# Performance work log

Hardware: AMD Instinct MI355X
Metric: run time of the kernel (lower is better)

The kernel has to match this reference:

```python
import jax, jax.numpy as jnp
import numpy as np

B, M, W, C, NN, J, ED, EMB = 8, 4096, 128, 32, 16, 4, 5, 2
EPS = 1e-5


def setup_inputs() -> dict:
    key = jax.random.key(0)
    ks = jax.random.split(key, 30)
    s = 0.05
    x = jax.random.normal(ks[0], (B, M, W), jnp.float32)
    pseudo = jax.random.normal(ks[1], (M * NN, EMB), jnp.float32)
    # structured indices: row r scatters its NN attention weights into row r of the m x m matrix
    nbr = jax.random.randint(ks[2], (M, NN), 0, M)
    L_idx = (jnp.arange(M)[:, None] * M + nbr).reshape(-1).astype(jnp.int32)
    inp = dict(x=x, pseudo=pseudo, L_idx=L_idx)
    inp['edge_w'] = jax.random.normal(ks[3], (ED, EMB), jnp.float32) * s
    inp['edge_b'] = jnp.zeros((ED,), jnp.float32)
    # Gaussian mixture params per layer (J components, encode_dim each); reset_parameters -> N(0,1)
    inp['mu0'] = jax.random.normal(ks[4], (J, ED), jnp.float32)
    inp['sigma0'] = jax.random.normal(ks[5], (J, ED), jnp.float32)
    inp['mu1'] = jax.random.normal(ks[6], (J, ED), jnp.float32)
    inp['sigma1'] = jax.random.normal(ks[7], (J, ED), jnp.float32)
    # layer 0: W -> C ; layer 1: C -> C
    inp['l1w0'] = jax.random.normal(ks[8], (C, W), jnp.float32) * s
    inp['l1b0'] = jnp.zeros((C,), jnp.float32)
    inp['l2w0'] = jax.random.normal(ks[9], (C, W), jnp.float32) * s
    inp['l2b0'] = jnp.zeros((C,), jnp.float32)
    inp['l1w1'] = jax.random.normal(ks[10], (C, C), jnp.float32) * s
    inp['l1b1'] = jnp.zeros((C,), jnp.float32)
    inp['l2w1'] = jax.random.normal(ks[11], (C, C), jnp.float32) * s
    inp['l2b1'] = jnp.zeros((C,), jnp.float32)
    inp['bn_g0'] = jnp.ones((C,), jnp.float32)
    inp['bn_b0'] = jnp.zeros((C,), jnp.float32)
    inp['bn_g1'] = jnp.ones((C,), jnp.float32)
    inp['bn_b1'] = jnp.zeros((C,), jnp.float32)
    inp['fc1w'] = jax.random.normal(ks[12], (256, M * C), jnp.float32) * 0.005
    inp['fc1b'] = jnp.zeros((256,), jnp.float32)
    inp['fc2w'] = jax.random.normal(ks[13], (53, 256), jnp.float32) * s
    inp['fc2b'] = jnp.zeros((53,), jnp.float32)
    return inp


def _get_L(pseudo, L_idx, edge_w, edge_b, mu, sigma, dtype):
    # Gaussian-mixture edge attention: u^T diag(sigma) u per component, summed, exp(-0.5 *)
    emb = pseudo @ edge_w.T + edge_b                      # (E, ED), E = M*NN
    u = emb[None, :, :] - mu[:, None, :]                  # (J, E, ED)
    q = jnp.sum(u * u * sigma[:, None, :], axis=-1)       # (J, E)
    w = jnp.sum(jnp.exp(-0.5 * q), axis=0)                # (E,)
    attn = jax.nn.softmax(w.reshape(M, NN), axis=1).reshape(-1)
    return jnp.zeros(M * M, dtype).at[L_idx].set(attn).reshape(M, M)


def _layer(x, L, w1, b1, w2, b2, g, bb):
    Lx = jnp.einsum('mn,bnf->bmf', L, x)                  # graph conv
    h = Lx @ w1.T + b1 + x @ w2.T + b2                    # (B, M, C)
    # BatchNorm1d (training mode): stats over batch and node dims, biased variance
    mean = jnp.mean(h, axis=(0, 1))
    var = jnp.var(h, axis=(0, 1))
    h = (h - mean) * jax.lax.rsqrt(var + EPS) * g + bb
    return jax.nn.relu(h)


def reference(x, pseudo, L_idx, edge_w, edge_b, mu0, sigma0, mu1, sigma1,
              l1w0, l1b0, l2w0, l2b0, l1w1, l1b1, l2w1, l2b1,
              bn_g0, bn_b0, bn_g1, bn_b1, fc1w, fc1b, fc2w, fc2b):
    L0 = _get_L(pseudo, L_idx, edge_w, edge_b, mu0, sigma0, x.dtype)
    h = _layer(x, L0, l1w0, l1b0, l2w0, l2b0, bn_g0, bn_b0)
    L1 = _get_L(pseudo, L_idx, edge_w, edge_b, mu1, sigma1, x.dtype)
    h = _layer(h, L1, l1w1, l1b1, l2w1, l2b1, bn_g1, bn_b1)
    flat = h.reshape(B, M * C)
    out = jax.nn.relu(flat @ fc1w.T + fc1b)               # dropout = identity (eval)
    return out @ fc2w.T + fc2b                            # (B, 53)
```

## Files before the change

### kernel.cpp

```cpp
#include <hip/hip_runtime.h>

#define B_ 8
#define M_ 4096
#define W_ 128
#define C_ 32
#define NN_ 16

typedef short s16x8 __attribute__((ext_vector_type(8)));
typedef float f32x4 __attribute__((ext_vector_type(4)));

static __device__ __forceinline__ unsigned short f2bf(float f) {
  unsigned u = __builtin_bit_cast(unsigned, f);
  u = u + 0x7FFFu + ((u >> 16) & 1u);
  return (unsigned short)(u >> 16);
}
static __device__ __forceinline__ s16x8 cvt8v(float4 a, float4 b) {
  s16x8 r;
  r[0] = (short)f2bf(a.x); r[1] = (short)f2bf(a.y);
  r[2] = (short)f2bf(a.z); r[3] = (short)f2bf(a.w);
  r[4] = (short)f2bf(b.x); r[5] = (short)f2bf(b.y);
  r[6] = (short)f2bf(b.z); r[7] = (short)f2bf(b.w);
  return r;
}
static __device__ __forceinline__ float safeexp(float a) {
  return expf(fminf(a, 87.f));
}

__global__ void poison_kernel(float* __restrict__ out, int n, float val) {
  int t = blockIdx.x * blockDim.x + threadIdx.x;
  if (t < n) out[t] = val;
}

__global__ __launch_bounds__(256) void init_kernel(
    float* __restrict__ fc1acc, const float* __restrict__ fc1b,
    float* __restrict__ bn) {
  int g = blockIdx.x * 256 + threadIdx.x;
  if (g < 2048) fc1acc[g] = fc1b[g & 255];
  else if (g < 34816) bn[g - 2048] = 0.f;
}

__global__ __launch_bounds__(256) void attn_kernel(
    const float* __restrict__ pseudo, const int* __restrict__ Lidx,
    const float* __restrict__ edge_w, const float* __restrict__ edge_b,
    const float* __restrict__ mu0, const float* __restrict__ sg0,
    const float* __restrict__ mu1, const float* __restrict__ sg1,
    float* __restrict__ we0, float* __restrict__ we1, int* __restrict__ colb) {
  int m = blockIdx.x * 256 + threadIdx.x;
  if (m >= M_) return;
  float w0[NN_], w1[NN_];
  int col[NN_];
#pragma unroll
  for (int n = 0; n < NN_; n++) {
    int e = m * NN_ + n;
    float p0 = pseudo[e * 2], p1 = pseudo[e * 2 + 1];
    float emb[5];
#pragma unroll
    for (int d = 0; d < 5; d++)
      emb[d] = p0 * edge_w[d * 2] + p1 * edge_w[d * 2 + 1] + edge_b[d];
    float a0 = 0.f, a1 = 0.f;
#pragma unroll
    for (int j = 0; j < 4; j++) {
      float qa = 0.f, qb = 0.f;
#pragma unroll
      for (int d = 0; d < 5; d++) {
        float u0 = emb[d] - mu0[j * 5 + d];
        qa += u0 * u0 * sg0[j * 5 + d];
        float u1 = emb[d] - mu1[j * 5 + d];
        qb += u1 * u1 * sg1[j * 5 + d];
      }
      a0 += safeexp(-0.5f * qa);
      a1 += safeexp(-0.5f * qb);
    }
    w0[n] = a0; w1[n] = a1;
    col[n] = Lidx[e] % M_;
  }
  float mx0 = w0[0], mx1 = w1[0];
#pragma unroll
  for (int n = 1; n < NN_; n++) { mx0 = fmaxf(mx0, w0[n]); mx1 = fmaxf(mx1, w1[n]); }
  float s0 = 0.f, s1 = 0.f;
#pragma unroll
  for (int n = 0; n < NN_; n++) {
    w0[n] = safeexp(w0[n] - mx0); s0 += w0[n];
    w1[n] = safeexp(w1[n] - mx1); s1 += w1[n];
  }
  float r0 = 1.f / s0, r1 = 1.f / s1;
#pragma unroll
  for (int n = 0; n < NN_; n++) {
    bool last = true;
#pragma unroll
    for (int n2 = n + 1; n2 < NN_; n2++)
      if (col[n2] == col[n]) last = false;
    int e = m * NN_ + n;
    we0[e] = last ? w0[n] * r0 : 0.f;
    we1[e] = last ? w1[n] * r1 : 0.f;
    colb[e] = col[n];
  }
}

__global__ __launch_bounds__(256) void proj0_kernel(
    const float* __restrict__ x, const float* __restrict__ l1w0,
    const float* __restrict__ l2w0, float* __restrict__ G) {
  int lane = threadIdx.x & 63, wave = threadIdx.x >> 6;
  int l16 = lane & 15, quad = lane >> 4;
  int tile = blockIdx.x * 4 + wave;
  s16x8 bf[4][4];
#pragma unroll
  for (int kit = 0; kit < 4; kit++) {
#pragma unroll
    for (int ct = 0; ct < 4; ct++) {
      int out = ct * 16 + l16;
      const float* src = (out < 32 ? l1w0 + out * 128 : l2w0 + (out - 32) * 128)
                         + kit * 32 + quad * 8;
      bf[kit][ct] = cvt8v(*(const float4*)src, *(const float4*)(src + 4));
    }
  }
  f32x4 acc[4];
#pragma unroll
  for (int ct = 0; ct < 4; ct++) acc[ct] = (f32x4){0.f, 0.f, 0.f, 0.f};
  int row = tile * 16 + l16;
  const float* xr = x + (size_t)row * 128 + quad * 8;
#pragma unroll
  for (int kit = 0; kit < 4; kit++) {
    const float* ap = xr + kit * 32;
    s16x8 a = cvt8v(*(const float4*)ap, *(const float4*)(ap + 4));
#pragma unroll
    for (int ct = 0; ct < 4; ct++)
      acc[ct] = __builtin_amdgcn_mfma_f32_16x16x32_bf16(a, bf[kit][ct], acc[ct], 0, 0, 0);
  }
  int rbase = tile * 16 + quad * 4;
#pragma unroll
  for (int ct = 0; ct < 4; ct++)
#pragma unroll
    for (int i = 0; i < 4; i++)
      G[(size_t)(rbase + i) * 64 + ct * 16 + l16] = acc[ct][i];
}

__global__ __launch_bounds__(256) void conv_kernel(
    const float* __restrict__ G,
    const float* __restrict__ we, const int* __restrict__ colb,
    const float* __restrict__ b1c, const float* __restrict__ b2c,
    float* __restrict__ h, float* __restrict__ bns, float* __restrict__ bnq) {
  __shared__ float s_we[8][16];
  __shared__ int   s_cn[8][16];
  __shared__ float s_s[32], s_q[32];
  int tid = threadIdx.x;
  if (tid < 128) {
    int row = tid >> 4, nn = tid & 15;
    int m = (blockIdx.x * 8 + row) & 4095;
    s_we[row][nn] = we[m * 16 + nn];
    s_cn[row][nn] = colb[m * 16 + nn];
  } else if (tid < 160) {
    s_s[tid - 128] = 0.f;
    s_q[tid - 128] = 0.f;
  }
  __syncthreads();
  int row = tid >> 5, c = tid & 31;
  int r = blockIdx.x * 8 + row;
  int b = r >> 12;
  const float* Gb = G + ((size_t)b << 18);
  float acc = 0.f;
#pragma unroll
  for (int nn = 0; nn < NN_; nn++)
    acc += s_we[row][nn] * Gb[s_cn[row][nn] * 64 + c];
  float hv = acc + G[(size_t)r * 64 + 32 + c] + b1c[c] + b2c[c];
  h[(size_t)r * 32 + c] = hv;
  atomicAdd(&s_s[c], hv);
  atomicAdd(&s_q[c], hv * hv);
  __syncthreads();
  if (tid < 32) {
    int slot = blockIdx.x & 255;
    atomicAdd(&bns[tid * 256 + slot], s_s[tid]);
    atomicAdd(&bnq[tid * 256 + slot], s_q[tid]);
  }
}

__global__ __launch_bounds__(256) void bnfin_kernel(
    const float* __restrict__ bns, const float* __restrict__ bnq,
    const float* __restrict__ g, const float* __restrict__ bb,
    float* __restrict__ scale, float* __restrict__ shift) {
  __shared__ float red[2][8][32];
  int tid = threadIdx.x;
  int c = tid & 31, part = tid >> 5;
  float s = 0.f, q = 0.f;
#pragma unroll 8
  for (int i = 0; i < 32; i++) {
    s += bns[c * 256 + part * 32 + i];
    q += bnq[c * 256 + part * 32 + i];
  }
  red[0][part][c] = s;
  red[1][part][c] = q;
  __syncthreads();
  if (tid < 32) {
    float S = 0.f, Q = 0.f;
#pragma unroll
    for (int p = 0; p < 8; p++) { S += red[0][p][tid]; Q += red[1][p][tid]; }
    float mean = S * (1.f / 32768.f);
    float var = fmaxf(Q * (1.f / 32768.f) - mean * mean, 0.f);
    float sc = g[tid] * rsqrtf(var + 1e-5f);
    scale[tid] = sc;
    shift[tid] = bb[tid] - mean * sc;
  }
}

__global__ __launch_bounds__(256) void proj1_kernel(
    const float* __restrict__ h0, const float* __restrict__ sc0,
    const float* __restrict__ l1w1, const float* __restrict__ l2w1,
    float* __restrict__ G) {
  int lane = threadIdx.x & 63, wave = threadIdx.x >> 6;
  int l16 = lane & 15, quad = lane >> 4;
  int tile = blockIdx.x * 4 + wave;
  s16x8 bf[4];
#pragma unroll
  for (int ct = 0; ct < 4; ct++) {
    int out = ct * 16 + l16;
    const float* src = (out < 32 ? l1w1 + out * 32 : l2w1 + (out - 32) * 32) + quad * 8;
    bf[ct] = cvt8v(*(const float4*)src, *(const float4*)(src + 4));
  }
  float scv[8], shv[8];
#pragma unroll
  for (int j = 0; j < 8; j++) {
    scv[j] = sc0[quad * 8 + j];
    shv[j] = sc0[32 + quad * 8 + j];
  }
  int row = tile * 16 + l16;
  const float* hr = h0 + (size_t)row * 32 + quad * 8;
  float4 hv0 = *(const float4*)hr;
  float4 hv1 = *(const float4*)(hr + 4);
  float av[8] = {hv0.x, hv0.y, hv0.z, hv0.w, hv1.x, hv1.y, hv1.z, hv1.w};
  s16x8 a;
#pragma unroll
  for (int j = 0; j < 8; j++)
    a[j] = (short)f2bf(fmaxf(av[j] * scv[j] + shv[j], 0.f));
  f32x4 acc[4];
#pragma unroll
  for (int ct = 0; ct < 4; ct++) {
    f32x4 z = {0.f, 0.f, 0.f, 0.f};
    acc[ct] = __builtin_amdgcn_mfma_f32_16x16x32_bf16(a, bf[ct], z, 0, 0, 0);
  }
  int rbase = tile * 16 + quad * 4;
#pragma unroll
  for (int ct = 0; ct < 4; ct++)
#pragma unroll
    for (int i = 0; i < 4; i++)
      G[(size_t)(rbase + i) * 64 + ct * 16 + l16] = acc[ct][i];
}

__global__ __launch_bounds__(256) void fc1_kernel(
    const float* __restrict__ h1, const float* __restrict__ sc1,
    const float* __restrict__ fc1w, float* __restrict__ fc1acc) {
  __shared__ short als[16 * 1024];
  int tid = threadIdx.x;
  int kc = blockIdx.x >> 2;
  int og = blockIdx.x & 3;
  size_t kbase = (size_t)kc << 10;
  for (int s = tid; s < 4096; s += 256) {
    int rowb = s >> 8;
    int k4 = (s & 255) << 2;
    short4 v4 = {0, 0, 0, 0};
    if (rowb < 8) {
      float4 hv = *(const float4*)(h1 + ((size_t)rowb << 17) + kbase + k4);
      int c = k4 & 31;
      float4 scv = *(const float4*)(sc1 + c);
      float4 shv = *(const float4*)(sc1 + 32 + c);
      v4.x = (short)f2bf(fmaxf(hv.x * scv.x + shv.x, 0.f));
      v4.y = (short)f2bf(fmaxf(hv.y * scv.y + shv.y, 0.f));
      v4.z = (short)f2bf(fmaxf(hv.z * scv.z + shv.z, 0.f));
      v4.w = (short)f2bf(fmaxf(hv.w * scv.w + shv.w, 0.f));
    }
    int byte = ((rowb << 11) + (k4 << 1)) ^ ((rowb & 7) << 4);
    *(short4*)((char*)als + byte) = v4;
  }
  __syncthreads();
  int lane = tid & 63, wave = tid >> 6;
  int l16 = lane & 15, quad = lane >> 4;
  const float* wrow = fc1w + (size_t)(og * 64 + wave * 16 + l16) * 131072
                      + kbase + quad * 8;
  int abase = (l16 << 11) + (quad << 4);
  int axor = (l16 & 7) << 4;
  f32x4 acc = {0.f, 0.f, 0.f, 0.f};
#pragma unroll 4
  for (int kk = 0; kk < 32; kk++) {
    const float* wp = wrow + kk * 32;
    s16x8 bfr = cvt8v(*(const float4*)wp, *(const float4*)(wp + 4));
    s16x8 afr = *(const s16x8*)((const char*)als + ((abase + (kk << 6)) ^ axor));
    acc = __builtin_amdgcn_mfma_f32_16x16x32_bf16(afr, bfr, acc, 0, 0, 0);
  }
  if (quad < 2) {
    int o = og * 64 + wave * 16 + l16;
#pragma unroll
    for (int i = 0; i < 4; i++)
      atomicAdd(&fc1acc[(quad * 4 + i) * 256 + o], acc[i]);
  }
}

__global__ void fc2_kernel(const float* __restrict__ fc1acc,
                           const float* __restrict__ fc2w,
                           const float* __restrict__ fc2b,
                           float* __restrict__ out) {
  int t = blockIdx.x * blockDim.x + threadIdx.x;
  if (t >= 424) return;
  int b = t / 53, j = t - b * 53;
  float s = fc2b[j];
  const float* fa = fc1acc + b * 256;
  const float* wr = fc2w + j * 256;
#pragma unroll 8
  for (int o = 0; o < 256; o++) s += fmaxf(fa[o], 0.f) * wr[o];
  out[t] = s;
}

extern "C" void kernel_launch(void* const* d_in, const int* in_sizes, int n_in,
                              void* d_out, int out_size, void* d_ws, size_t ws_size,
                              hipStream_t stream) {
  float* out = (float*)d_out;
  int bad = 0;
  if (n_in != 25) bad = 2;
  else if (in_sizes[0] != 4194304) bad = 3;
  else if (in_sizes[2] != 65536) bad = 4;
  else if (in_sizes[21] != 33554432) bad = 5;
  else if (out_size != 424) bad = 6;
  else if (ws_size < 13509120) bad = 1;
  if (bad) {
    poison_kernel<<<2, 256, 0, stream>>>(out, out_size, (float)bad * 1.0e6f);
    return;
  }

  const float* x      = (const float*)d_in[0];
  const float* pseudo = (const float*)d_in[1];
  const int*   Lidx   = (const int*)d_in[2];
  const float* edge_w = (const float*)d_in[3];
  const float* edge_b = (const float*)d_in[4];
  const float* mu0    = (const float*)d_in[5];
  const float* sg0    = (const float*)d_in[6];
  const float* mu1    = (const float*)d_in[7];
  const float* sg1    = (const float*)d_in[8];
  const float* l1w0   = (const float*)d_in[9];
  const float* l1b0   = (const float*)d_in[10];
  const float* l2w0   = (const float*)d_in[11];
  const float* l2b0   = (const float*)d_in[12];
  const float* l1w1   = (const float*)d_in[13];
  const float* l1b1   = (const float*)d_in[14];
  const float* l2w1   = (const float*)d_in[15];
  const float* l2b1   = (const float*)d_in[16];
  const float* bng0   = (const float*)d_in[17];
  const float* bnb0   = (const float*)d_in[18];
  const float* bng1   = (const float*)d_in[19];
  const float* bnb1   = (const float*)d_in[20];
  const float* fc1w   = (const float*)d_in[21];
  const float* fc1b   = (const float*)d_in[22];
  const float* fc2w   = (const float*)d_in[23];
  const float* fc2b   = (const float*)d_in[24];

  char* Wp = (char*)d_ws;
  int*   colb   = (int*)  (Wp + 0);
  float* we0    = (float*)(Wp + 262144);
  float* we1    = (float*)(Wp + 524288);
  float* G      = (float*)(Wp + 786432);
  float* h0     = (float*)(Wp + 9175040);
  float* h1     = (float*)(Wp + 9175040);
  float* bn     = (float*)(Wp + 13369344);
  float* sc     = (float*)(Wp + 13500416);
  float* fc1acc = (float*)(Wp + 13500928);

  init_kernel<<<136, 256, 0, stream>>>(fc1acc, fc1b, bn);
  attn_kernel<<<16, 256, 0, stream>>>(pseudo, Lidx, edge_w, edge_b,
                                      mu0, sg0, mu1, sg1, we0, we1, colb);
  proj0_kernel<<<512, 256, 0, stream>>>(x, l1w0, l2w0, G);
  conv_kernel<<<4096, 256, 0, stream>>>(G, we0, colb, l1b0, l2b0,
                                        h0, bn, bn + 8192);
  bnfin_kernel<<<1, 256, 0, stream>>>(bn, bn + 8192, bng0, bnb0, sc, sc + 32);
  proj1_kernel<<<512, 256, 0, stream>>>(h0, sc, l1w1, l2w1, G);
  conv_kernel<<<4096, 256, 0, stream>>>(G, we1, colb, l1b1, l2b1,
                                        h1, bn + 16384, bn + 24576);
  bnfin_kernel<<<1, 256, 0, stream>>>(bn + 16384, bn + 24576, bng1, bnb1,
                                      sc + 64, sc + 96);
  fc1_kernel<<<512, 256, 0, stream>>>(h1, sc + 64, fc1w, fc1acc);
  fc2_kernel<<<2, 256, 0, stream>>>(fc1acc, fc2w, fc2b, out);
}
```

Measured before the change: 346.5 us.

## Fuse init/attn/proj0, fold BN finalize into consumers, prefetch fc1 weights, split fc1 K

Merges the init, attention and layer-0 projection kernels into one launch, and folds each BatchNorm finalize into the kernel that consumes it. Each block now recomputes the scale and shift redundantly, which removes the single-block kernels and their launch gaps. The second conv kernel also reads the whole 128 MB fc1 weight array through an empty asm sink so it lands in cache (L2/MALL) before fc1 runs. fc1 now uses twice as many blocks, each splitting K across wave pairs and combining them through LDS. The risks are extra memory traffic from the prefetch and repeated BN reductions in every block.

```diff
diff --git a/kernel.cpp b/kernel.cpp
--- a/kernel.cpp
+++ b/kernel.cpp
@@ -31,22 +31,13 @@
   if (t < n) out[t] = val;
 }
 
-__global__ __launch_bounds__(256) void init_kernel(
-    float* __restrict__ fc1acc, const float* __restrict__ fc1b,
-    float* __restrict__ bn) {
-  int g = blockIdx.x * 256 + threadIdx.x;
-  if (g < 2048) fc1acc[g] = fc1b[g & 255];
-  else if (g < 34816) bn[g - 2048] = 0.f;
-}
-
-__global__ __launch_bounds__(256) void attn_kernel(
-    const float* __restrict__ pseudo, const int* __restrict__ Lidx,
+
+static __device__ void attn_row(
+    int m, const float* __restrict__ pseudo, const int* __restrict__ Lidx,
     const float* __restrict__ edge_w, const float* __restrict__ edge_b,
     const float* __restrict__ mu0, const float* __restrict__ sg0,
     const float* __restrict__ mu1, const float* __restrict__ sg1,
     float* __restrict__ we0, float* __restrict__ we1, int* __restrict__ colb) {
-  int m = blockIdx.x * 256 + threadIdx.x;
-  if (m >= M_) return;
   float w0[NN_], w1[NN_];
   int col[NN_];
 #pragma unroll
@@ -97,35 +88,29 @@
   }
 }
 
-__global__ __launch_bounds__(256) void proj0_kernel(
-    const float* __restrict__ x, const float* __restrict__ l1w0,
+static __device__ void proj0_tile(
+    int blk, int tid, const float* __restrict__ x, const float* __restrict__ l1w0,
     const float* __restrict__ l2w0, float* __restrict__ G) {
-  int lane = threadIdx.x & 63, wave = threadIdx.x >> 6;
+  int lane = tid & 63, wave = tid >> 6;
   int l16 = lane & 15, quad = lane >> 4;
-  int tile = blockIdx.x * 4 + wave;
-  s16x8 bf[4][4];
+  int tile = blk * 4 + wave;
+  f32x4 acc[4];
+#pragma unroll
+  for (int ct = 0; ct < 4; ct++) acc[ct] = (f32x4){0.f, 0.f, 0.f, 0.f};
+  int row = tile * 16 + l16;
+  const float* xr = x + (size_t)row * 128 + quad * 8;
 #pragma unroll
   for (int kit = 0; kit < 4; kit++) {
+    const float* ap = xr + kit * 32;
+    s16x8 a = cvt8v(*(const float4*)ap, *(const float4*)(ap + 4));
 #pragma unroll
     for (int ct = 0; ct < 4; ct++) {
       int out = ct * 16 + l16;
       const float* src = (out < 32 ? l1w0 + out * 128 : l2w0 + (out - 32) * 128)
                          + kit * 32 + quad * 8;
-      bf[kit][ct] = cvt8v(*(const float4*)src, *(const float4*)(src + 4));
+      s16x8 bf = cvt8v(*(const float4*)src, *(const float4*)(src + 4));
+      acc[ct] = __builtin_amdgcn_mfma_f32_16x16x32_bf16(a, bf, acc[ct], 0, 0, 0);
     }
-  }
-  f32x4 acc[4];
-#pragma unroll
-  for (int ct = 0; ct < 4; ct++) acc[ct] = (f32x4){0.f, 0.f, 0.f, 0.f};
-  int row = tile * 16 + l16;
-  const float* xr = x + (size_t)row * 128 + quad * 8;
-#pragma unroll
-  for (int kit = 0; kit < 4; kit++) {
-    const float* ap = xr + kit * 32;
-    s16x8 a = cvt8v(*(const float4*)ap, *(const float4*)(ap + 4));
-#pragma unroll
-    for (int ct = 0; ct < 4; ct++)
-      acc[ct] = __builtin_amdgcn_mfma_f32_16x16x32_bf16(a, bf[kit][ct], acc[ct], 0, 0, 0);
   }
   int rbase = tile * 16 + quad * 4;
 #pragma unroll
@@ -135,18 +120,19 @@
       G[(size_t)(rbase + i) * 64 + ct * 16 + l16] = acc[ct][i];
 }
 
-__global__ __launch_bounds__(256) void conv_kernel(
-    const float* __restrict__ G,
-    const float* __restrict__ we, const int* __restrict__ colb,
-    const float* __restrict__ b1c, const float* __restrict__ b2c,
-    float* __restrict__ h, float* __restrict__ bns, float* __restrict__ bnq) {
-  __shared__ float s_we[8][16];
-  __shared__ int   s_cn[8][16];
-  __shared__ float s_s[32], s_q[32];
-  int tid = threadIdx.x;
+static __device__ void conv_block(
+    int cb, int tid, char* smem,
+    const float* __restrict__ G, const float* __restrict__ we,
+    const int* __restrict__ colb, const float* __restrict__ b1c,
+    const float* __restrict__ b2c, float* __restrict__ h,
+    float* __restrict__ bns, float* __restrict__ bnq) {
+  float (*s_we)[16] = (float(*)[16])smem;
+  int   (*s_cn)[16] = (int(*)[16])(smem + 512);
+  float* s_s = (float*)(smem + 1024);
+  float* s_q = (float*)(smem + 1152);
   if (tid < 128) {
     int row = tid >> 4, nn = tid & 15;
-    int m = (blockIdx.x * 8 + row) & 4095;
+    int m = (cb * 8 + row) & 4095;
     s_we[row][nn] = we[m * 16 + nn];
     s_cn[row][nn] = colb[m * 16 + nn];
   } else if (tid < 160) {
@@ -155,7 +141,7 @@
   }
   __syncthreads();
   int row = tid >> 5, c = tid & 31;
-  int r = blockIdx.x * 8 + row;
+  int r = cb * 8 + row;
   int b = r >> 12;
   const float* Gb = G + ((size_t)b << 18);
   float acc = 0.f;
@@ -168,18 +154,17 @@
   atomicAdd(&s_q[c], hv * hv);
   __syncthreads();
   if (tid < 32) {
-    int slot = blockIdx.x & 255;
+    int slot = cb & 255;
     atomicAdd(&bns[tid * 256 + slot], s_s[tid]);
     atomicAdd(&bnq[tid * 256 + slot], s_q[tid]);
   }
 }
 
-__global__ __launch_bounds__(256) void bnfin_kernel(
-    const float* __restrict__ bns, const float* __restrict__ bnq,
+static __device__ void bnfin_local(
+    int tid, char* smem, const float* __restrict__ bns, const float* __restrict__ bnq,
     const float* __restrict__ g, const float* __restrict__ bb,
-    float* __restrict__ scale, float* __restrict__ shift) {
-  __shared__ float red[2][8][32];
-  int tid = threadIdx.x;
+    float* __restrict__ s_sc) {
+  float (*red)[8][32] = (float(*)[8][32])smem;
   int c = tid & 31, part = tid >> 5;
   float s = 0.f, q = 0.f;
 #pragma unroll 8
@@ -197,31 +182,19 @@
     float mean = S * (1.f / 32768.f);
     float var = fmaxf(Q * (1.f / 32768.f) - mean * mean, 0.f);
     float sc = g[tid] * rsqrtf(var + 1e-5f);
-    scale[tid] = sc;
-    shift[tid] = bb[tid] - mean * sc;
-  }
-}
-
-__global__ __launch_bounds__(256) void proj1_kernel(
-    const float* __restrict__ h0, const float* __restrict__ sc0,
+    s_sc[tid] = sc;
+    s_sc[32 + tid] = bb[tid] - mean * sc;
+  }
+  __syncthreads();
+}
+
+static __device__ void proj1_tile(
+    int blk, int tid, const float* __restrict__ h0, const float* __restrict__ sc0,
     const float* __restrict__ l1w1, const float* __restrict__ l2w1,
     float* __restrict__ G) {
-  int lane = threadIdx.x & 63, wave = threadIdx.x >> 6;
+  int lane = tid & 63, wave = tid >> 6;
   int l16 = lane & 15, quad = lane >> 4;
-  int tile = blockIdx.x * 4 + wave;
-  s16x8 bf[4];
-#pragma unroll
-  for (int ct = 0; ct < 4; ct++) {
-    int out = ct * 16 + l16;
-    const float* src = (out < 32 ? l1w1 + out * 32 : l2w1 + (out - 32) * 32) + quad * 8;
-    bf[ct] = cvt8v(*(const float4*)src, *(const float4*)(src + 4));
-  }
-  float scv[8], shv[8];
-#pragma unroll
-  for (int j = 0; j < 8; j++) {
-    scv[j] = sc0[quad * 8 + j];
-    shv[j] = sc0[32 + quad * 8 + j];
-  }
+  int tile = blk * 4 + wave;
   int row = tile * 16 + l16;
   const float* hr = h0 + (size_t)row * 32 + quad * 8;
   float4 hv0 = *(const float4*)hr;
@@ -229,13 +202,19 @@
   float av[8] = {hv0.x, hv0.y, hv0.z, hv0.w, hv1.x, hv1.y, hv1.z, hv1.w};
   s16x8 a;
 #pragma unroll
-  for (int j = 0; j < 8; j++)
-    a[j] = (short)f2bf(fmaxf(av[j] * scv[j] + shv[j], 0.f));
+  for (int j = 0; j < 8; j++) {
+    float scv = sc0[quad * 8 + j];
+    float shv = sc0[32 + quad * 8 + j];
+    a[j] = (short)f2bf(fmaxf(av[j] * scv + shv, 0.f));
+  }
   f32x4 acc[4];
 #pragma unroll
   for (int ct = 0; ct < 4; ct++) {
+    int out = ct * 16 + l16;
+    const float* src = (out < 32 ? l1w1 + out * 32 : l2w1 + (out - 32) * 32) + quad * 8;
+    s16x8 bf = cvt8v(*(const float4*)src, *(const float4*)(src + 4));
     f32x4 z = {0.f, 0.f, 0.f, 0.f};
-    acc[ct] = __builtin_amdgcn_mfma_f32_16x16x32_bf16(a, bf[ct], z, 0, 0, 0);
+    acc[ct] = __builtin_amdgcn_mfma_f32_16x16x32_bf16(a, bf, z, 0, 0, 0);
   }
   int rbase = tile * 16 + quad * 4;
 #pragma unroll
@@ -245,13 +224,94 @@
       G[(size_t)(rbase + i) * 64 + ct * 16 + l16] = acc[ct][i];
 }
 
-__global__ __launch_bounds__(256) void fc1_kernel(
-    const float* __restrict__ h1, const float* __restrict__ sc1,
+static __device__ void fc2_elem(
+    int t, const float* __restrict__ fc1acc, const float* __restrict__ fc2w,
+    const float* __restrict__ fc2b, float* __restrict__ out) {
+  int b = t / 53, j = t - b * 53;
+  float s = fc2b[j];
+  const float* fa = fc1acc + b * 256;
+  const float* wr = fc2w + j * 256;
+#pragma unroll 8
+  for (int o = 0; o < 256; o++) s += fmaxf(fa[o], 0.f) * wr[o];
+  out[t] = s;
+}
+
+
+__global__ __launch_bounds__(256) void k1_kernel(
+    const float* __restrict__ x, const float* __restrict__ l1w0,
+    const float* __restrict__ l2w0, float* __restrict__ G,
+    const float* __restrict__ pseudo, const int* __restrict__ Lidx,
+    const float* __restrict__ edge_w, const float* __restrict__ edge_b,
+    const float* __restrict__ mu0, const float* __restrict__ sg0,
+    const float* __restrict__ mu1, const float* __restrict__ sg1,
+    float* __restrict__ we0, float* __restrict__ we1, int* __restrict__ colb,
+    float* __restrict__ fc1acc, const float* __restrict__ fc1b,
+    float* __restrict__ bn) {
+  int bid = blockIdx.x, tid = threadIdx.x;
+  if (bid < 512) {
+    proj0_tile(bid, tid, x, l1w0, l2w0, G);
+  } else if (bid < 528) {
+    attn_row((bid - 512) * 256 + tid, pseudo, Lidx, edge_w, edge_b,
+             mu0, sg0, mu1, sg1, we0, we1, colb);
+  } else {
+    int g = (bid - 528) * 256 + tid;
+    if (g < 2048) fc1acc[g] = fc1b[g & 255];
+    else bn[g - 2048] = 0.f;
+  }
+}
+
+__global__ __launch_bounds__(256) void conv_kernel(
+    const float* __restrict__ G,
+    const float* __restrict__ we, const int* __restrict__ colb,
+    const float* __restrict__ b1c, const float* __restrict__ b2c,
+    float* __restrict__ h, float* __restrict__ bns, float* __restrict__ bnq) {
+  __shared__ char smem[1280];
+  conv_block(blockIdx.x, threadIdx.x, smem, G, we, colb, b1c, b2c, h, bns, bnq);
+}
+
+__global__ __launch_bounds__(256) void proj1bn_kernel(
+    const float* __restrict__ h0,
+    const float* __restrict__ bns, const float* __restrict__ bnq,
+    const float* __restrict__ g0, const float* __restrict__ b0,
+    const float* __restrict__ l1w1, const float* __restrict__ l2w1,
+    float* __restrict__ G) {
+  __shared__ char smem[2048];
+  __shared__ __align__(16) float s_sc[64];
+  bnfin_local(threadIdx.x, smem, bns, bnq, g0, b0, s_sc);
+  proj1_tile(blockIdx.x, threadIdx.x, h0, s_sc, l1w1, l2w1, G);
+}
+
+__global__ __launch_bounds__(256) void conv_pf_kernel(
+    const float* __restrict__ G,
+    const float* __restrict__ we, const int* __restrict__ colb,
+    const float* __restrict__ b1c, const float* __restrict__ b2c,
+    float* __restrict__ h, float* __restrict__ bns, float* __restrict__ bnq,
+    const float* __restrict__ fc1w) {
+  __shared__ char smem[1280];
+  conv_block(blockIdx.x, threadIdx.x, smem, G, we, colb, b1c, b2c, h, bns, bnq);
+  const float4* pw = (const float4*)fc1w;
+  int base = blockIdx.x * 2048 + threadIdx.x;
+  float a = 0.f;
+#pragma unroll
+  for (int j = 0; j < 8; j++) {
+    float4 v = pw[base + j * 256];
+    a += v.x + v.y + v.z + v.w;
+  }
+  asm volatile("" :: "v"(a));
+}
+
+__global__ __launch_bounds__(256) void fc1bn_kernel(
+    const float* __restrict__ h1,
+    const float* __restrict__ bns, const float* __restrict__ bnq,
+    const float* __restrict__ g1, const float* __restrict__ b1,
     const float* __restrict__ fc1w, float* __restrict__ fc1acc) {
-  __shared__ short als[16 * 1024];
+  __shared__ char smem[32768];
+  __shared__ __align__(16) float s_sc[64];
   int tid = threadIdx.x;
-  int kc = blockIdx.x >> 2;
-  int og = blockIdx.x & 3;
+  bnfin_local(tid, smem, bns, bnq, g1, b1, s_sc);
+  short* als = (short*)smem;
+  int kc = blockIdx.x >> 3;
+  int og = blockIdx.x & 7;
   size_t kbase = (size_t)kc << 10;
   for (int s = tid; s < 4096; s += 256) {
     int rowb = s >> 8;
@@ -260,8 +320,8 @@
     if (rowb < 8) {
       float4 hv = *(const float4*)(h1 + ((size_t)rowb << 17) + kbase + k4);
       int c = k4 & 31;
-      float4 scv = *(const float4*)(sc1 + c);
-      float4 shv = *(const float4*)(sc1 + 32 + c);
+      float4 scv = *(const float4*)(s_sc + c);
+      float4 shv = *(const float4*)(s_sc + 32 + c);
       v4.x = (short)f2bf(fmaxf(hv.x * scv.x + shv.x, 0.f));
       v4.y = (short)f2bf(fmaxf(hv.y * scv.y + shv.y, 0.f));
       v4.z = (short)f2bf(fmaxf(hv.z * scv.z + shv.z, 0.f));
@@ -273,23 +333,32 @@
   __syncthreads();
   int lane = tid & 63, wave = tid >> 6;
   int l16 = lane & 15, quad = lane >> 4;
-  const float* wrow = fc1w + (size_t)(og * 64 + wave * 16 + l16) * 131072
-                      + kbase + quad * 8;
-  int abase = (l16 << 11) + (quad << 4);
+  int p = wave >> 1, khalf = wave & 1;
+  int o = og * 32 + p * 16 + l16;
+  const float* wr = fc1w + (size_t)o * 131072 + kbase + (khalf << 9) + quad * 8;
+  int abase = (l16 << 11) + (khalf << 10) + (quad << 4);
   int axor = (l16 & 7) << 4;
   f32x4 acc = {0.f, 0.f, 0.f, 0.f};
 #pragma unroll 4
-  for (int kk = 0; kk < 32; kk++) {
-    const float* wp = wrow + kk * 32;
+  for (int kk = 0; kk < 16; kk++) {
+    const float* wp = wr + kk * 32;
     s16x8 bfr = cvt8v(*(const float4*)wp, *(const float4*)(wp + 4));
     s16x8 afr = *(const s16x8*)((const char*)als + ((abase + (kk << 6)) ^ axor));
     acc = __builtin_amdgcn_mfma_f32_16x16x32_bf16(afr, bfr, acc, 0, 0, 0);
   }
-  if (quad < 2) {
-    int o = og * 64 + wave * 16 + l16;
+  __syncthreads();
+  float* red = (float*)smem;
+  if (khalf == 1 && quad < 2) {
 #pragma unroll
     for (int i = 0; i < 4; i++)
-      atomicAdd(&fc1acc[(quad * 4 + i) * 256 + o], acc[i]);
+      red[(p * 8 + quad * 4 + i) * 16 + l16] = acc[i];
+  }
+  __syncthreads();
+  if (khalf == 0 && quad < 2) {
+#pragma unroll
+    for (int i = 0; i < 4; i++)
+      atomicAdd(&fc1acc[(quad * 4 + i) * 256 + o],
+                acc[i] + red[(p * 8 + quad * 4 + i) * 16 + l16]);
   }
 }
 
@@ -298,14 +367,7 @@
                            const float* __restrict__ fc2b,
                            float* __restrict__ out) {
   int t = blockIdx.x * blockDim.x + threadIdx.x;
-  if (t >= 424) return;
-  int b = t / 53, j = t - b * 53;
-  float s = fc2b[j];
-  const float* fa = fc1acc + b * 256;
-  const float* wr = fc2w + j * 256;
-#pragma unroll 8
-  for (int o = 0; o < 256; o++) s += fmaxf(fa[o], 0.f) * wr[o];
-  out[t] = s;
+  if (t < 424) fc2_elem(t, fc1acc, fc2w, fc2b, out);
 }
 
 extern "C" void kernel_launch(void* const* d_in, const int* in_sizes, int n_in,
@@ -356,23 +418,19 @@
   float* we1    = (float*)(Wp + 524288);
   float* G      = (float*)(Wp + 786432);
   float* h0     = (float*)(Wp + 9175040);
-  float* h1     = (float*)(Wp + 9175040);
   float* bn     = (float*)(Wp + 13369344);
-  float* sc     = (float*)(Wp + 13500416);
   float* fc1acc = (float*)(Wp + 13500928);
 
-  init_kernel<<<136, 256, 0, stream>>>(fc1acc, fc1b, bn);
-  attn_kernel<<<16, 256, 0, stream>>>(pseudo, Lidx, edge_w, edge_b,
-                                      mu0, sg0, mu1, sg1, we0, we1, colb);
-  proj0_kernel<<<512, 256, 0, stream>>>(x, l1w0, l2w0, G);
+  k1_kernel<<<664, 256, 0, stream>>>(x, l1w0, l2w0, G, pseudo, Lidx,
+                                     edge_w, edge_b, mu0, sg0, mu1, sg1,
+                                     we0, we1, colb, fc1acc, fc1b, bn);
   conv_kernel<<<4096, 256, 0, stream>>>(G, we0, colb, l1b0, l2b0,
                                         h0, bn, bn + 8192);
-  bnfin_kernel<<<1, 256, 0, stream>>>(bn, bn + 8192, bng0, bnb0, sc, sc + 32);
-  proj1_kernel<<<512, 256, 0, stream>>>(h0, sc, l1w1, l2w1, G);
-  conv_kernel<<<4096, 256, 0, stream>>>(G, we1, colb, l1b1, l2b1,
-                                        h1, bn + 16384, bn + 24576);
-  bnfin_kernel<<<1, 256, 0, stream>>>(bn + 16384, bn + 24576, bng1, bnb1,
-                                      sc + 64, sc + 96);
-  fc1_kernel<<<512, 256, 0, stream>>>(h1, sc + 64, fc1w, fc1acc);
+  proj1bn_kernel<<<512, 256, 0, stream>>>(h0, bn, bn + 8192, bng0, bnb0,
+                                          l1w1, l2w1, G);
+  conv_pf_kernel<<<4096, 256, 0, stream>>>(G, we1, colb, l1b1, l2b1,
+                                           h0, bn + 16384, bn + 24576, fc1w);
+  fc1bn_kernel<<<1024, 256, 0, stream>>>(h0, bn + 16384, bn + 24576,
+                                         bng1, bnb1, fc1w, fc1acc);
   fc2_kernel<<<2, 256, 0, stream>>>(fc1acc, fc2w, fc2b, out);
 }
```

After: 341.4 us. No clear change (-1.5%).
